# Kernel optimization log

Measured on AMD Instinct MI355X. Metric: run time of the kernel, lower is better.

The kernel has to match this reference:

```python
import jax, jax.numpy as jnp
import numpy as np

B, N, D, D_OUT = 8, 2048, 1024, 1024

def setup_inputs() -> dict:
    key = jax.random.key(0)
    k1, k2, k3, k4, k5 = jax.random.split(key, 5)
    x = jax.random.normal(k1, (B, N, D), dtype=jnp.float32)
    # nn.Linear params: weight [out, in], bias [out]
    W_attn = jax.random.normal(k2, (D, D), dtype=jnp.float32) / np.sqrt(D)
    b_attn = jax.random.normal(k3, (D,), dtype=jnp.float32) * 0.01
    W_out = jax.random.normal(k4, (D_OUT, D), dtype=jnp.float32) / np.sqrt(D)
    b_out = jax.random.normal(k5, (D_OUT,), dtype=jnp.float32) * 0.01
    return {"x": x, "W_attn": W_attn, "b_attn": b_attn, "W_out": W_out, "b_out": b_out}

def reference(x, W_attn, b_attn, W_out, b_out):
    # query = x; key = attention_linear(x); value = output_linear(x)
    key = jnp.einsum('bnd,kd->bnk', x, W_attn) + b_attn   # [B,N,D]
    value = jnp.einsum('bnd,od->bno', x, W_out) + b_out   # [B,N,D_OUT]
    scale = 1.0 / np.sqrt(x.shape[-1]).astype(np.float32)
    scores = jnp.einsum('bqd,bkd->bqk', x, key) * scale   # [B,N,N]
    attn = jax.nn.softmax(scores, axis=-1)
    return jnp.einsum('bqk,bko->bqo', attn, value)        # [B,N,D_OUT]
```

## Files before the change

### kernel.cpp

```cpp
#include <hip/hip_runtime.h>
#include <hip/hip_bf16.h>
#include <cstdio>

typedef __bf16 bf16_t;
typedef __bf16 bf16x8 __attribute__((ext_vector_type(8)));
typedef __bf16 bf16x4 __attribute__((ext_vector_type(4)));
typedef float  f32x16 __attribute__((ext_vector_type(16)));

#define TILE_E (256 * 64)

__global__ __launch_bounds__(256)
void cvt_all(const float* __restrict__ x,  bf16_t* __restrict__ xb,  int nX,
             const float* __restrict__ Wa, bf16_t* __restrict__ Wab,
             const float* __restrict__ Wo, bf16_t* __restrict__ Wob, int nW)
{
    const int nT = nX + 2 * nW;
    for (int i = (blockIdx.x * 256 + threadIdx.x) * 4; i < nT; i += gridDim.x * 256 * 4) {
        const float* src; bf16_t* dst; int off;
        if (i < nX)            { src = x;  dst = xb;  off = i; }
        else if (i < nX + nW)  { src = Wa; dst = Wab; off = i - nX; }
        else                   { src = Wo; dst = Wob; off = i - nX - nW; }
        const float4 v = *(const float4*)(src + off);
        bf16x4 o;
        o[0] = (bf16_t)v.x; o[1] = (bf16_t)v.y; o[2] = (bf16_t)v.z; o[3] = (bf16_t)v.w;
        *(bf16x4*)(dst + off) = o;
    }
}


template<int K>
__device__ __forceinline__ void stage_half(
    const bf16_t* __restrict__ src, bf16_t* lds_tile,
    int half, int kt, int w, int l)
{
    const int r0 = half * 128 + w * 8 + (l >> 3);
    const int c8 = ((l & 7) ^ (l >> 3) ^ ((w & 3) << 1)) * 8;
#pragma unroll
    for (int rr = 0; rr < 2; rr++) {
        __builtin_amdgcn_global_load_lds(
            (const __attribute__((address_space(1))) void*)
                (src + (size_t)(r0 + rr * 64) * K + (size_t)kt * 64 + c8),
            (__attribute__((address_space(3))) void*)
                (lds_tile + (half * 128 + rr * 64 + w * 8) * 64),
            16, 0, 0);
    }
}

#define RDF_A(f, ks) (*(const bf16x8*)&sAc[(aoff + (f) * 32 + l31) * 64 + ((((ks) * 2 + l5) ^ swz) * 8)])
#define RDF_B(f, ks) (*(const bf16x8*)&sBc[(boff + (f) * 32 + l31) * 64 + ((((ks) * 2 + l5) ^ swz) * 8)])

#define MFMA_Q(AR, BV, MB, NB)                                             \
    _Pragma("unroll") for (int ks = 0; ks < 4; ks++)                       \
    _Pragma("unroll") for (int mi = 0; mi < 2; mi++)                       \
        acc[(MB) + mi][NB] = __builtin_amdgcn_mfma_f32_32x32x16_bf16(      \
            AR[mi][ks], BV[ks], acc[(MB) + mi][NB], 0, 0, 0);

#define LGKM0_FENCE                                        \
    asm volatile("s_waitcnt lgkmcnt(0)" ::: "memory");     \
    __builtin_amdgcn_sched_barrier(0);

template<int K>
__device__ __forceinline__ void gemm256_core(
    const bf16_t* __restrict__ Ab, const bf16_t* __restrict__ Bb,
    f32x16 (&acc)[4][2], int w, int l, int wm, int wn)
{
    __shared__ bf16_t sA[2 * TILE_E];
    __shared__ bf16_t sB[2 * TILE_E];
    constexpr int NKT = K / 64;

    const int l31 = l & 31, l5 = l >> 5;
    const int swz = (l & 7) ^ ((l >> 2) & 6);
    const int aoff = wm * 128, boff = wn * 64;

    stage_half<K>(Ab, sA, 0, 0, w, l);
    stage_half<K>(Bb, sB, 0, 0, w, l);
    stage_half<K>(Ab, sA, 1, 0, w, l);
    stage_half<K>(Bb, sB, 1, 0, w, l);
    asm volatile("s_waitcnt vmcnt(0)" ::: "memory");
    __builtin_amdgcn_s_barrier();

    bf16x8 arA[2][4], arB[2][4], bl[4], bh[4];

    for (int t = 0; t < NKT; ++t) {
        bf16_t* sAc = sA + (t & 1) * TILE_E;
        bf16_t* sBc = sB + (t & 1) * TILE_E;
        bf16_t* sAn = sA + ((t + 1) & 1) * TILE_E;
        bf16_t* sBn = sB + ((t + 1) & 1) * TILE_E;
        const bool pf = (t + 1 < NKT);

#pragma unroll
        for (int mi = 0; mi < 2; mi++)
#pragma unroll
            for (int ks = 0; ks < 4; ks++) arA[mi][ks] = RDF_A(mi, ks);
#pragma unroll
        for (int ks = 0; ks < 4; ks++) bl[ks] = RDF_B(0, ks);
        if (pf) {
            stage_half<K>(Ab, sAn, 0, t + 1, w, l);
            stage_half<K>(Bb, sBn, 0, t + 1, w, l);
        }
        asm volatile("s_waitcnt lgkmcnt(8)" ::: "memory");
        __builtin_amdgcn_s_barrier();
        LGKM0_FENCE
        __builtin_amdgcn_s_setprio(1);
        MFMA_Q(arA, bl, 0, 0)
        __builtin_amdgcn_s_setprio(0);
        __builtin_amdgcn_s_barrier();

#pragma unroll
        for (int ks = 0; ks < 4; ks++) bh[ks] = RDF_B(1, ks);
        if (pf) {
            stage_half<K>(Ab, sAn, 1, t + 1, w, l);
            stage_half<K>(Bb, sBn, 1, t + 1, w, l);
        }
        __builtin_amdgcn_s_barrier();
        LGKM0_FENCE
        __builtin_amdgcn_s_setprio(1);
        MFMA_Q(arA, bh, 0, 1)
        __builtin_amdgcn_s_setprio(0);
        __builtin_amdgcn_s_barrier();

#pragma unroll
        for (int mi = 0; mi < 2; mi++)
#pragma unroll
            for (int ks = 0; ks < 4; ks++) arB[mi][ks] = RDF_A(2 + mi, ks);
        __builtin_amdgcn_s_barrier();
        LGKM0_FENCE
        __builtin_amdgcn_s_setprio(1);
        MFMA_Q(arB, bl, 2, 0)
        __builtin_amdgcn_s_setprio(0);
        __builtin_amdgcn_s_barrier();

        __builtin_amdgcn_s_setprio(1);
        MFMA_Q(arB, bh, 2, 1)
        __builtin_amdgcn_s_setprio(0);
        if (pf) {
            asm volatile("s_waitcnt vmcnt(0)" ::: "memory");
            __builtin_amdgcn_s_barrier();
        }
    }
}

#define ACC_INIT(acc)                                            \
    _Pragma("unroll") for (int i = 0; i < 4; i++)                \
    _Pragma("unroll") for (int j = 0; j < 2; j++)                \
    _Pragma("unroll") for (int e = 0; e < 16; e++) acc[i][j][e] = 0.f;

__global__ __launch_bounds__(512, 2)
void gemm_kv8(const bf16_t* __restrict__ xb,
              const bf16_t* __restrict__ Wa, const bf16_t* __restrict__ Wo,
              const float* __restrict__ ba, const float* __restrict__ bo,
              bf16_t* __restrict__ key, bf16_t* __restrict__ vT)
{
    constexpr int K = 1024, Nn = 2048, Dd = 1024;
    const int tid = threadIdx.x;
    const int w = tid >> 6, l = tid & 63;
    const int wm = w >> 2, wn = w & 3;

    const int bid = blockIdx.x;
    const int id  = (bid & 7) * 64 + (bid >> 3);
    const int b   = id >> 6;
    const int rest = id & 63;
    const int tm  = rest & 7;
    const int tn  = rest >> 3;
    const bool isK = tn < 4;

    const bf16_t* Ab = xb + (size_t)b * Nn * K + (size_t)tm * 256 * K;
    const bf16_t* Bb = isK ? (Wa + (size_t)tn * 256 * K)
                           : (Wo + (size_t)(tn - 4) * 256 * K);

    f32x16 acc[4][2];
    ACC_INIT(acc)
    gemm256_core<K>(Ab, Bb, acc, w, l, wm, wn);

    const int l31 = l & 31, l5 = l >> 5;
    if (isK) {
#pragma unroll
        for (int n = 0; n < 2; n++) {
            const int cg = (tn & 3) * 256 + wn * 64 + n * 32 + l31;
            const float bv = ba[cg];
#pragma unroll
            for (int m = 0; m < 4; m++)
#pragma unroll
                for (int rg = 0; rg < 4; rg++) {
                    const int rowg = tm * 256 + wm * 128 + m * 32 + rg * 8 + 4 * l5;
                    bf16_t* p = key + (size_t)b * Nn * Dd + (size_t)rowg * Dd + cg;
#pragma unroll
                    for (int j = 0; j < 4; j++)
                        p[(size_t)j * Dd] = (bf16_t)(acc[m][n][rg * 4 + j] + bv);
                }
        }
    } else {
#pragma unroll
        for (int n = 0; n < 2; n++) {
            const int cg = (tn & 3) * 256 + wn * 64 + n * 32 + l31;
            const float bv = bo[cg];
#pragma unroll
            for (int m = 0; m < 4; m++)
#pragma unroll
                for (int rg = 0; rg < 4; rg++) {
                    const int rowg = tm * 256 + wm * 128 + m * 32 + rg * 8 + 4 * l5;
                    bf16x4 pk;
#pragma unroll
                    for (int j = 0; j < 4; j++) pk[j] = (bf16_t)(acc[m][n][rg * 4 + j] + bv);
                    *(bf16x4*)(vT + (size_t)b * Dd * Nn + (size_t)cg * Nn + rowg) = pk;
                }
        }
    }
}

__global__ __launch_bounds__(512, 2)
void gemm_scores8(const bf16_t* __restrict__ xb, const bf16_t* __restrict__ key,
                  bf16_t* __restrict__ S)
{
    constexpr int K = 1024, Nn = 2048;
    const int tid = threadIdx.x;
    const int w = tid >> 6, l = tid & 63;
    const int wm = w >> 2, wn = w & 3;

    const int bid = blockIdx.x;
    const int id  = (bid & 7) * 64 + (bid >> 3);
    const int b   = id >> 6;
    const int rest = id & 63;
    const int tm  = rest & 7;
    const int tn  = rest >> 3;

    const bf16_t* Ab = xb  + (size_t)b * Nn * K + (size_t)tm * 256 * K;
    const bf16_t* Bb = key + (size_t)b * Nn * K + (size_t)tn * 256 * K;

    f32x16 acc[4][2];
    ACC_INIT(acc)
    gemm256_core<K>(Ab, Bb, acc, w, l, wm, wn);

    const int l31 = l & 31, l5 = l >> 5;
#pragma unroll
    for (int n = 0; n < 2; n++) {
        const int cg = tn * 256 + wn * 64 + n * 32 + l31;
#pragma unroll
        for (int m = 0; m < 4; m++)
#pragma unroll
            for (int rg = 0; rg < 4; rg++) {
                const int rowg = tm * 256 + wm * 128 + m * 32 + rg * 8 + 4 * l5;
                bf16_t* p = S + (size_t)b * Nn * Nn + (size_t)rowg * Nn + cg;
#pragma unroll
                for (int j = 0; j < 4; j++)
                    p[(size_t)j * Nn] = (bf16_t)(acc[m][n][rg * 4 + j] * 0.03125f);
            }
    }
}

__global__ __launch_bounds__(256)
void softmax_rows(bf16_t* __restrict__ S)
{
    __shared__ float red[8];
    const int t = threadIdx.x;
    const int w = t >> 6;
    const int lane = t & 63;
    bf16_t* p = S + (size_t)blockIdx.x * 2048;

    bf16x8 v = *(const bf16x8*)&p[t * 8];
    float x[8];
    float m = -1e30f;
#pragma unroll
    for (int i = 0; i < 8; i++) { x[i] = (float)v[i]; m = fmaxf(m, x[i]); }
#pragma unroll
    for (int off = 32; off >= 1; off >>= 1) m = fmaxf(m, __shfl_xor(m, off));
    if (lane == 0) red[w] = m;
    __syncthreads();
    m = fmaxf(fmaxf(red[0], red[1]), fmaxf(red[2], red[3]));

    float s = 0.f;
#pragma unroll
    for (int i = 0; i < 8; i++) { x[i] = __expf(x[i] - m); s += x[i]; }
#pragma unroll
    for (int off = 32; off >= 1; off >>= 1) s += __shfl_xor(s, off);
    if (lane == 0) red[4 + w] = s;
    __syncthreads();
    const float inv = 1.f / (red[4] + red[5] + red[6] + red[7]);

    bf16x8 o;
#pragma unroll
    for (int i = 0; i < 8; i++) o[i] = (bf16_t)(x[i] * inv);
    *(bf16x8*)&p[t * 8] = o;
}

__global__ __launch_bounds__(512, 2)
void gemm_out8(const bf16_t* __restrict__ P, const bf16_t* __restrict__ vT,
               float* __restrict__ out)
{
    constexpr int K = 2048, Nn = 2048, Dd = 1024;
    const int tid = threadIdx.x;
    const int w = tid >> 6, l = tid & 63;
    const int wm = w >> 2, wn = w & 3;

    const int bid = blockIdx.x;
    const int id  = (bid & 7) * 32 + (bid >> 3);
    const int b   = id >> 5;
    const int rest = id & 31;
    const int tm  = rest & 7;
    const int tn  = rest >> 3;

    const bf16_t* Ab = P  + (size_t)b * Nn * Nn + (size_t)tm * 256 * Nn;
    const bf16_t* Bb = vT + (size_t)b * Dd * Nn + (size_t)tn * 256 * Nn;

    f32x16 acc[4][2];
    ACC_INIT(acc)
    gemm256_core<K>(Ab, Bb, acc, w, l, wm, wn);

    const int l31 = l & 31, l5 = l >> 5;
#pragma unroll
    for (int n = 0; n < 2; n++) {
        const int cg = tn * 256 + wn * 64 + n * 32 + l31;
#pragma unroll
        for (int m = 0; m < 4; m++)
#pragma unroll
            for (int rg = 0; rg < 4; rg++) {
                const int rowg = tm * 256 + wm * 128 + m * 32 + rg * 8 + 4 * l5;
                float* p = out + (size_t)b * Nn * Dd + (size_t)rowg * Dd + cg;
#pragma unroll
                for (int j = 0; j < 4; j++)
                    p[(size_t)j * Dd] = acc[m][n][rg * 4 + j];
            }
    }
}

extern "C" void kernel_launch(void* const* d_in, const int* in_sizes, int n_in,
                              void* d_out, int out_size, void* d_ws, size_t ws_size,
                              hipStream_t stream)
{
    const int Bn = 8, Nn = 2048, Dd = 1024;

    const float* x  = (const float*)d_in[0];
    const float* Wa = (const float*)d_in[1];
    const float* ba = (const float*)d_in[2];
    const float* Wo = (const float*)d_in[3];
    const float* bo = (const float*)d_in[4];
    float* out = (float*)d_out;

    const size_t nX = (size_t)Bn * Nn * Dd;
    const size_t nW = (size_t)Dd * Dd;
    const size_t nS = (size_t)Bn * Nn * Nn;

    bf16_t* xb  = (bf16_t*)d_ws;
    bf16_t* Wab = xb + nX;
    bf16_t* Wob = Wab + nW;
    bf16_t* key = Wob + nW;
    bf16_t* vT  = key + nX;
    bf16_t* S   = vT + nX;
    const size_t needed = (nX * 3 + nW * 2 + nS) * sizeof(bf16_t);
    if (ws_size < needed)
        fprintf(stderr, "kernel_launch: ws too small: have %zu need %zu\n", ws_size, needed);

    cvt_all<<<dim3(18432), dim3(256), 0, stream>>>(x, xb, (int)nX, Wa, Wab, Wo, Wob, (int)nW);

    gemm_kv8<<<dim3(512), dim3(512), 0, stream>>>(xb, Wab, Wob, ba, bo, key, vT);

    gemm_scores8<<<dim3(512), dim3(512), 0, stream>>>(xb, key, S);

    softmax_rows<<<dim3(Bn * Nn), dim3(256), 0, stream>>>(S);

    gemm_out8<<<dim3(256), dim3(512), 0, stream>>>(S, vT, out);
}
```

Baseline: 370.0 us.

## Fuse softmax into score GEMM epilogue and defer normalization to output GEMM

Removes the standalone row-softmax kernel. The scores GEMM epilogue now writes exp(score) directly to S and emits per-tile partial row sums to a small workspace. The output GEMM sums those partials into per-row inverse sums in shared memory and scales its accumulators at store time. This avoids a full extra read and write of the B×N×N score matrix and one kernel launch. The cost is that the row max is no longer subtracted, so exp can overflow or lose bf16 precision if scores get large.

```diff
diff --git a/kernel.cpp b/kernel.cpp
--- a/kernel.cpp
+++ b/kernel.cpp
@@ -210,7 +210,7 @@
 
 __global__ __launch_bounds__(512, 2)
 void gemm_scores8(const bf16_t* __restrict__ xb, const bf16_t* __restrict__ key,
-                  bf16_t* __restrict__ S)
+                  bf16_t* __restrict__ S, float* __restrict__ rowpart)
 {
     constexpr int K = 1024, Nn = 2048;
     const int tid = threadIdx.x;
@@ -233,61 +233,50 @@
 
     const int l31 = l & 31, l5 = l >> 5;
 #pragma unroll
-    for (int n = 0; n < 2; n++) {
-        const int cg = tn * 256 + wn * 64 + n * 32 + l31;
-#pragma unroll
-        for (int m = 0; m < 4; m++)
+    for (int m = 0; m < 4; m++) {
+        float part[4][4];
+#pragma unroll
+        for (int rg = 0; rg < 4; rg++)
+#pragma unroll
+            for (int j = 0; j < 4; j++) part[rg][j] = 0.f;
+#pragma unroll
+        for (int n = 0; n < 2; n++) {
+            const int cg = tn * 256 + wn * 64 + n * 32 + l31;
 #pragma unroll
             for (int rg = 0; rg < 4; rg++) {
                 const int rowg = tm * 256 + wm * 128 + m * 32 + rg * 8 + 4 * l5;
                 bf16_t* p = S + (size_t)b * Nn * Nn + (size_t)rowg * Nn + cg;
 #pragma unroll
-                for (int j = 0; j < 4; j++)
-                    p[(size_t)j * Nn] = (bf16_t)(acc[m][n][rg * 4 + j] * 0.03125f);
+                for (int j = 0; j < 4; j++) {
+                    const float e = __expf(acc[m][n][rg * 4 + j] * 0.03125f);
+                    part[rg][j] += e;
+                    p[(size_t)j * Nn] = (bf16_t)e;
+                }
             }
-    }
-}
-
-__global__ __launch_bounds__(256)
-void softmax_rows(bf16_t* __restrict__ S)
-{
-    __shared__ float red[8];
-    const int t = threadIdx.x;
-    const int w = t >> 6;
-    const int lane = t & 63;
-    bf16_t* p = S + (size_t)blockIdx.x * 2048;
-
-    bf16x8 v = *(const bf16x8*)&p[t * 8];
-    float x[8];
-    float m = -1e30f;
-#pragma unroll
-    for (int i = 0; i < 8; i++) { x[i] = (float)v[i]; m = fmaxf(m, x[i]); }
-#pragma unroll
-    for (int off = 32; off >= 1; off >>= 1) m = fmaxf(m, __shfl_xor(m, off));
-    if (lane == 0) red[w] = m;
-    __syncthreads();
-    m = fmaxf(fmaxf(red[0], red[1]), fmaxf(red[2], red[3]));
-
-    float s = 0.f;
-#pragma unroll
-    for (int i = 0; i < 8; i++) { x[i] = __expf(x[i] - m); s += x[i]; }
-#pragma unroll
-    for (int off = 32; off >= 1; off >>= 1) s += __shfl_xor(s, off);
-    if (lane == 0) red[4 + w] = s;
-    __syncthreads();
-    const float inv = 1.f / (red[4] + red[5] + red[6] + red[7]);
-
-    bf16x8 o;
-#pragma unroll
-    for (int i = 0; i < 8; i++) o[i] = (bf16_t)(x[i] * inv);
-    *(bf16x8*)&p[t * 8] = o;
+        }
+#pragma unroll
+        for (int rg = 0; rg < 4; rg++)
+#pragma unroll
+            for (int j = 0; j < 4; j++) {
+                float v = part[rg][j];
+#pragma unroll
+                for (int off = 16; off >= 1; off >>= 1)
+                    v += __shfl_xor(v, off);
+                if (l31 == 0) {
+                    const int rowg = tm * 256 + wm * 128 + m * 32 + rg * 8 + 4 * l5 + j;
+                    rowpart[((size_t)b * 2048 + rowg) * 32 + tn * 4 + wn] = v;
+                }
+            }
+    }
 }
 
 __global__ __launch_bounds__(512, 2)
 void gemm_out8(const bf16_t* __restrict__ P, const bf16_t* __restrict__ vT,
-               float* __restrict__ out)
+               const float* __restrict__ rowpart, float* __restrict__ out)
 {
     constexpr int K = 2048, Nn = 2048, Dd = 1024;
+    __shared__ float invS[256];
+
     const int tid = threadIdx.x;
     const int w = tid >> 6, l = tid & 63;
     const int wm = w >> 2, wn = w & 3;
@@ -299,6 +288,14 @@
     const int tm  = rest & 7;
     const int tn  = rest >> 3;
 
+    if (tid < 256) {
+        const float* rp = rowpart + ((size_t)b * 2048 + tm * 256 + tid) * 32;
+        float s = 0.f;
+#pragma unroll
+        for (int i = 0; i < 32; i++) s += rp[i];
+        invS[tid] = 1.f / s;
+    }
+
     const bf16_t* Ab = P  + (size_t)b * Nn * Nn + (size_t)tm * 256 * Nn;
     const bf16_t* Bb = vT + (size_t)b * Dd * Nn + (size_t)tn * 256 * Nn;
 
@@ -314,11 +311,11 @@
         for (int m = 0; m < 4; m++)
 #pragma unroll
             for (int rg = 0; rg < 4; rg++) {
-                const int rowg = tm * 256 + wm * 128 + m * 32 + rg * 8 + 4 * l5;
-                float* p = out + (size_t)b * Nn * Dd + (size_t)rowg * Dd + cg;
+                const int rl = wm * 128 + m * 32 + rg * 8 + 4 * l5;
+                float* p = out + (size_t)b * Nn * Dd + (size_t)(tm * 256 + rl) * Dd + cg;
 #pragma unroll
                 for (int j = 0; j < 4; j++)
-                    p[(size_t)j * Dd] = acc[m][n][rg * 4 + j];
+                    p[(size_t)j * Dd] = acc[m][n][rg * 4 + j] * invS[rl + j];
             }
     }
 }
@@ -339,6 +336,7 @@
     const size_t nX = (size_t)Bn * Nn * Dd;
     const size_t nW = (size_t)Dd * Dd;
     const size_t nS = (size_t)Bn * Nn * Nn;
+    const size_t nR = (size_t)Bn * 2048 * 32;
 
     bf16_t* xb  = (bf16_t*)d_ws;
     bf16_t* Wab = xb + nX;
@@ -346,7 +344,8 @@
     bf16_t* key = Wob + nW;
     bf16_t* vT  = key + nX;
     bf16_t* S   = vT + nX;
-    const size_t needed = (nX * 3 + nW * 2 + nS) * sizeof(bf16_t);
+    float* rowpart = (float*)(S + nS);
+    const size_t needed = (nX * 3 + nW * 2 + nS) * sizeof(bf16_t) + nR * sizeof(float);
     if (ws_size < needed)
         fprintf(stderr, "kernel_launch: ws too small: have %zu need %zu\n", ws_size, needed);
 
@@ -354,9 +353,7 @@
 
     gemm_kv8<<<dim3(512), dim3(512), 0, stream>>>(xb, Wab, Wob, ba, bo, key, vT);
 
-    gemm_scores8<<<dim3(512), dim3(512), 0, stream>>>(xb, key, S);
-
-    softmax_rows<<<dim3(Bn * Nn), dim3(256), 0, stream>>>(S);
-
-    gemm_out8<<<dim3(256), dim3(512), 0, stream>>>(S, vT, out);
-}
+    gemm_scores8<<<dim3(512), dim3(512), 0, stream>>>(xb, key, S, rowpart);
+
+    gemm_out8<<<dim3(256), dim3(512), 0, stream>>>(S, vT, rowpart, out);
+}
```

Result: no change. 363.4 us (-1.8%).
